# Kernel optimization log

Hardware: AMD Instinct MI355X
Metric: run time of the kernel (lower is better)

## Reference

```python
import jax, jax.numpy as jnp
import numpy as np

SCALE = 0.08838834764831845  # 1/sqrt(128)
SOFT_CAP = 0.0               # module default soft_cap=0 -> disabled


def setup_inputs() -> dict:
    key = jax.random.key(0)
    k1, k2, k3, k4, k5 = jax.random.split(key, 5)
    R, B, Hq, Hk, Dq, Dv = 4, 16, 32, 8, 128, 128
    P, PAGE, M = 8192, 1, 2048  # pages per rank, page_size, max pages per seq
    q = jax.random.normal(k1, (B, Hq, Dq), dtype=jnp.float16)
    k_cache = jax.random.normal(k2, (R, P, PAGE, Hk, Dq), dtype=jnp.float16)
    v_cache = jax.random.normal(k3, (R, P, PAGE, Hk, Dv), dtype=jnp.float16)
    # at least 1 valid token per rank per sequence
    global_kv_lens = jax.random.randint(k4, (R, B), 1, M * PAGE + 1, dtype=jnp.int32)
    block_table = jax.random.randint(k5, (R, B, M), 0, P, dtype=jnp.int32)
    return {"q": q, "k_cache": k_cache, "v_cache": v_cache,
            "global_kv_lens": global_kv_lens, "block_table": block_table}


def _flash_decode(q, k_cache, v_cache, global_kv_lens, block_table):
    R, P, PAGE, Hk, Dq = k_cache.shape
    B, Hq, _ = q.shape
    G = Hq // Hk                      # GQA group size
    M = block_table.shape[-1]
    K = M * PAGE                      # max kv tokens per rank per seq
    Dv = v_cache.shape[-1]

    # paged gather per rank: kc[bt] -> [B, M, PAGE, Hk, D]
    kg = jax.vmap(lambda kc, bt: kc[bt])(k_cache, block_table)
    vg = jax.vmap(lambda vc, bt: vc[bt])(v_cache, block_table)
    kg = kg.reshape(R, B, K, Hk, Dq).astype(jnp.float32)
    vg = vg.reshape(R, B, K, Hk, Dv).astype(jnp.float32)

    qf = q.astype(jnp.float32).reshape(B, Hk, G, Dq)
    # scores [R, B, Hk, G, K]
    s = jnp.einsum('bhgd,rbkhd->rbhgk', qf, kg) * SCALE
    if SOFT_CAP > 0:
        s = SOFT_CAP * jnp.tanh(s / SOFT_CAP)

    valid = jnp.arange(K)[None, None, :] < global_kv_lens[:, :, None]  # [R,B,K]
    s = jnp.where(valid[:, :, None, None, :], s, -jnp.inf)

    # per-rank partial softmax stats (what gqa_local_kernels_fused produces)
    m = jnp.max(s, axis=-1)                      # [R,B,Hk,G]
    p = jnp.exp(s - m[..., None])
    l = jnp.sum(p, axis=-1)                      # [R,B,Hk,G]
    o = jnp.einsum('rbhgk,rbkhd->rbhgd', p, vg)  # [R,B,Hk,G,Dv]

    # cross-rank lse-weighted reduce (gqa_global_reduce_fused)
    m_g = jnp.max(m, axis=0)                     # [B,Hk,G]
    w = jnp.exp(m - m_g[None])                   # [R,B,Hk,G]
    o_tot = jnp.sum(w[..., None] * o, axis=0)    # [B,Hk,G,Dv]
    l_tot = jnp.sum(w * l, axis=0)               # [B,Hk,G]
    out = (o_tot / l_tot[..., None]).reshape(B, Hq, Dv)
    return out.astype(jnp.float32)


def reference(q, k_cache, v_cache, global_kv_lens, block_table):
    return _flash_decode(q, k_cache, v_cache, global_kv_lens, block_table)
```

## Files before the change

### kernel.cpp

```cpp
#include <hip/hip_runtime.h>
#include <math.h>


typedef float f32x4 __attribute__((ext_vector_type(4)));

#define R_ 4
#define B_ 16
#define HQ_ 32
#define HK_ 8
#define G_ 4
#define D_ 128
#define P_ 8192
#define M_ 2048
#define HKD (HK_ * D_)
#define SC2 (0.08838834764831845f * 1.4426950408889634f)
#define MNEG (-1.0e30f)

__device__ __forceinline__ void load8u(const float* __restrict__ ubase,
                                       unsigned boff, float o[8]) {
  const f32x4* p = (const f32x4*)((const char*)ubase + boff);
  f32x4 a = p[0];
  f32x4 b = p[1];
#pragma unroll
  for (int j = 0; j < 4; ++j) { o[j] = a[j]; o[4 + j] = b[j]; }
}

__device__ __forceinline__ int clampP(int p) {
  return p < 0 ? 0 : (p >= P_ ? P_ - 1 : p);
}

__global__ __launch_bounds__(256) void fd_partial(
    const float* __restrict__ q, const float* __restrict__ kc,
    const float* __restrict__ vc, const int* __restrict__ lens,
    const int* __restrict__ bt, float* __restrict__ ws_m,
    float* __restrict__ ws_l, float* __restrict__ ws_o, int S) {
  const int idx = blockIdx.x;
  const int s = idx % S;
  const int hk = (idx / S) % HK_;
  const int b = (idx / (S * HK_)) % B_;
  const int r = idx / (S * HK_ * B_);

  const int lane = threadIdx.x & 63;
  const int w = threadIdx.x >> 6;
  const int tg = lane >> 4;
  const int ds = (lane & 15) * 8;
  const unsigned dsb = ds * 4u;
  const int rec = blockIdx.x;

  int kvlen = lens[r * B_ + b];
  if (kvlen < 0) kvlen = 0;
  if (kvlen > M_) kvlen = M_;
  const int chunk = (((kvlen + S - 1) / S) + 63) & ~63;
  const int t0 = s * chunk;
  int t1 = t0 + chunk;
  if (t1 > kvlen) t1 = kvlen;
  if (t0 >= t1) {
    if (lane == 0) ws_m[rec * G_ + w] = MNEG;
    return;
  }

  float qf[G_][8];
  {
    const float* qp = q + (size_t)(b * HQ_ + hk * G_) * D_ + ds;
#pragma unroll
    for (int h = 0; h < G_; ++h) {
      load8u(qp + h * D_, 0u, qf[h]);
#pragma unroll
      for (int j = 0; j < 8; ++j) qf[h][j] *= SC2;
    }
  }

  const int* btrow = bt + (r * B_ + b) * M_;
  const float* kb = kc + (size_t)r * P_ * HKD + (size_t)hk * D_;
  const float* vb = vc + (size_t)r * P_ * HKD + (size_t)hk * D_;

  float m[G_], l[G_], acc[G_][8];
#pragma unroll
  for (int h = 0; h < G_; ++h) {
    m[h] = MNEG;
    l[h] = 0.f;
#pragma unroll
    for (int j = 0; j < 8; ++j) acc[h][j] = 0.f;
  }

  const int nIter = (t1 - t0 + 63) >> 6;
  const int sbase = t0 + w * 16 + tg * 4;

  int4 pgN = *(const int4*)(btrow + sbase);

  for (int i = 0; i < nIter; ++i) {
    const int4 pg = pgN;
    if (i + 1 < nIter) pgN = *(const int4*)(btrow + sbase + (i + 1) * 64);
    const unsigned o0 = ((unsigned)clampP(pg.x) << 12) + dsb;
    const unsigned o1 = ((unsigned)clampP(pg.y) << 12) + dsb;
    const unsigned o2 = ((unsigned)clampP(pg.z) << 12) + dsb;
    const unsigned o3 = ((unsigned)clampP(pg.w) << 12) + dsb;

    float k0[8], k1[8], k2[8], k3[8], v0[8], v1[8], v2[8], v3[8];
    load8u(kb, o0, k0);
    load8u(kb, o1, k1);
    load8u(kb, o2, k2);
    load8u(kb, o3, k3);
    load8u(vb, o0, v0);
    load8u(vb, o1, v1);
    load8u(vb, o2, v2);
    load8u(vb, o3, v3);

    float d0[G_], d1[G_], d2[G_], d3[G_];
#pragma unroll
    for (int h = 0; h < G_; ++h) {
      float a0 = 0.f, a1 = 0.f, a2 = 0.f, a3 = 0.f;
#pragma unroll
      for (int j = 0; j < 8; ++j) {
        a0 += qf[h][j] * k0[j];
        a1 += qf[h][j] * k1[j];
        a2 += qf[h][j] * k2[j];
        a3 += qf[h][j] * k3[j];
      }
      d0[h] = a0; d1[h] = a1; d2[h] = a2; d3[h] = a3;
    }
#pragma unroll
    for (int msk = 1; msk <= 8; msk <<= 1) {
#pragma unroll
      for (int h = 0; h < G_; ++h) {
        d0[h] += __shfl_xor(d0[h], msk);
        d1[h] += __shfl_xor(d1[h], msk);
        d2[h] += __shfl_xor(d2[h], msk);
        d3[h] += __shfl_xor(d3[h], msk);
      }
    }

    const int tb = sbase + i * 64;
    const bool va0 = tb < t1;
    const bool va1 = tb + 1 < t1;
    const bool va2 = tb + 2 < t1;
    const bool va3 = tb + 3 < t1;
#pragma unroll
    for (int h = 0; h < G_; ++h) {
      const float s0 = va0 ? d0[h] : -INFINITY;
      const float s1 = va1 ? d1[h] : -INFINITY;
      const float s2 = va2 ? d2[h] : -INFINITY;
      const float s3 = va3 ? d3[h] : -INFINITY;
      const float mt = fmaxf(fmaxf(s0, s1), fmaxf(s2, s3));
      const float mn = fmaxf(m[h], mt);
      const float sc = exp2f(m[h] - mn);
      const float p0 = exp2f(s0 - mn);
      const float p1 = exp2f(s1 - mn);
      const float p2 = exp2f(s2 - mn);
      const float p3 = exp2f(s3 - mn);
      m[h] = mn;
      l[h] = l[h] * sc + (p0 + p1) + (p2 + p3);
#pragma unroll
      for (int j = 0; j < 8; ++j)
        acc[h][j] = acc[h][j] * sc + p0 * v0[j] + p1 * v1[j] + p2 * v2[j] +
                    p3 * v3[j];
    }
  }

#pragma unroll
  for (int h = 0; h < G_; ++h) {
#pragma unroll
    for (int off = 16; off <= 32; off <<= 1) {
      const float mo = __shfl_xor(m[h], off);
      const float lo = __shfl_xor(l[h], off);
      float ao[8];
#pragma unroll
      for (int j = 0; j < 8; ++j) ao[j] = __shfl_xor(acc[h][j], off);
      const float mn = fmaxf(m[h], mo);
      const float se = exp2f(m[h] - mn);
      const float so_ = exp2f(mo - mn);
      l[h] = l[h] * se + lo * so_;
#pragma unroll
      for (int j = 0; j < 8; ++j) acc[h][j] = acc[h][j] * se + ao[j] * so_;
      m[h] = mn;
    }
  }

  __shared__ float sm[4][G_], sl[4][G_], so[4][G_][D_ + 4];
  if (lane < 16) {
#pragma unroll
    for (int h = 0; h < G_; ++h) {
#pragma unroll
      for (int j = 0; j < 8; ++j) so[w][h][ds + j] = acc[h][j];
    }
    if (lane == 0) {
#pragma unroll
      for (int h = 0; h < G_; ++h) {
        sm[w][h] = m[h];
        sl[w][h] = l[h];
      }
    }
  }
  __syncthreads();

  const int g = w;
  const float mw0 = sm[0][g], mw1 = sm[1][g], mw2 = sm[2][g], mw3 = sm[3][g];
  const float mf = fmaxf(fmaxf(mw0, mw1), fmaxf(mw2, mw3));
  const float wt0 = exp2f(mw0 - mf);
  const float wt1 = exp2f(mw1 - mf);
  const float wt2 = exp2f(mw2 - mf);
  const float wt3 = exp2f(mw3 - mf);
  const float lf =
      wt0 * sl[0][g] + wt1 * sl[1][g] + wt2 * sl[2][g] + wt3 * sl[3][g];
  const float of0 = wt0 * so[0][g][lane] + wt1 * so[1][g][lane] +
                    wt2 * so[2][g][lane] + wt3 * so[3][g][lane];
  const float of1 = wt0 * so[0][g][lane + 64] + wt1 * so[1][g][lane + 64] +
                    wt2 * so[2][g][lane + 64] + wt3 * so[3][g][lane + 64];
  ws_o[((size_t)rec * G_ + g) * D_ + lane] = of0;
  ws_o[((size_t)rec * G_ + g) * D_ + lane + 64] = of1;
  if (lane == 0) {
    ws_m[rec * G_ + g] = mf;
    ws_l[rec * G_ + g] = lf;
  }
}

__global__ __launch_bounds__(128) void fd_reduce(
    const float* __restrict__ ws_m, const float* __restrict__ ws_l,
    const float* __restrict__ ws_o, float* __restrict__ out, int S) {
  const int row = blockIdx.x;
  const int g = row % G_;
  const int hk = (row / G_) % HK_;
  const int b = row / (G_ * HK_);
  const int d = threadIdx.x;

  float mf = MNEG;
  for (int r = 0; r < R_; ++r)
    for (int s = 0; s < S; ++s) {
      int rec = ((r * B_ + b) * HK_ + hk) * S + s;
      mf = fmaxf(mf, ws_m[rec * G_ + g]);
    }
  float of = 0.f, lf = 0.f;
  for (int r = 0; r < R_; ++r)
    for (int s = 0; s < S; ++s) {
      int rec = ((r * B_ + b) * HK_ + hk) * S + s;
      float wt = exp2f(ws_m[rec * G_ + g] - mf);
      of += wt * ws_o[((size_t)rec * G_ + g) * D_ + d];
      lf += wt * ws_l[rec * G_ + g];
    }
  out[(size_t)(b * HQ_ + hk * G_ + g) * D_ + d] = of / lf;
}

__global__ __launch_bounds__(256) void fd_mono(
    const float* __restrict__ q, const float* __restrict__ kc,
    const float* __restrict__ vc, const int* __restrict__ lens,
    const int* __restrict__ bt, float* __restrict__ out) {
  const int hk = blockIdx.x % HK_;
  const int b = blockIdx.x / HK_;
  const int lane = threadIdx.x & 63;
  const int g = threadIdx.x >> 6;
  const int tg = lane >> 4;
  const int ds = (lane & 15) * 8;
  const unsigned dsb = ds * 4u;

  float qf[8];
  load8u(q + (size_t)(b * HQ_ + hk * G_ + g) * D_ + ds, 0u, qf);
#pragma unroll
  for (int j = 0; j < 8; ++j) qf[j] *= SC2;

  float m = MNEG, l = 0.f, acc[8];
#pragma unroll
  for (int j = 0; j < 8; ++j) acc[j] = 0.f;

  for (int r = 0; r < R_; ++r) {
    int kvlen = lens[r * B_ + b];
    if (kvlen < 0) kvlen = 0;
    if (kvlen > M_) kvlen = M_;
    const int* btrow = bt + (r * B_ + b) * M_;
    const float* kb = kc + (size_t)r * P_ * HKD + (size_t)hk * D_;
    const float* vb = vc + (size_t)r * P_ * HKD + (size_t)hk * D_;

    for (int t = 0; t < kvlen; t += 4) {
      const int ta = t + tg;
      const bool va = ta < kvlen;
      const unsigned oa = ((unsigned)clampP(btrow[va ? ta : 0]) << 12) + dsb;
      float ka[8], wa[8];
      load8u(kb, oa, ka);
      load8u(vb, oa, wa);

      float da = 0.f;
#pragma unroll
      for (int j = 0; j < 8; ++j) da += qf[j] * ka[j];
#pragma unroll
      for (int msk = 1; msk <= 8; msk <<= 1) da += __shfl_xor(da, msk);

      const float sa = va ? da : -INFINITY;
      const float mn = fmaxf(m, sa);
      const float sc = exp2f(m - mn);
      const float pa = exp2f(sa - mn);
      m = mn;
      l = l * sc + pa;
#pragma unroll
      for (int j = 0; j < 8; ++j) acc[j] = acc[j] * sc + pa * wa[j];
    }
  }

#pragma unroll
  for (int off = 16; off <= 32; off <<= 1) {
    const float mo = __shfl_xor(m, off);
    const float lo = __shfl_xor(l, off);
    float ao[8];
#pragma unroll
    for (int j = 0; j < 8; ++j) ao[j] = __shfl_xor(acc[j], off);
    const float mn = fmaxf(m, mo);
    const float se = exp2f(m - mn);
    const float so_ = exp2f(mo - mn);
    l = l * se + lo * so_;
#pragma unroll
    for (int j = 0; j < 8; ++j) acc[j] = acc[j] * se + ao[j] * so_;
    m = mn;
  }

  if (lane < 16) {
    float inv = (l > 0.f) ? 1.0f / l : 0.f;
#pragma unroll
    for (int j = 0; j < 8; ++j)
      out[(size_t)(b * HQ_ + hk * G_ + g) * D_ + ds + j] = acc[j] * inv;
  }
}

extern "C" void kernel_launch(void* const* d_in, const int* in_sizes, int n_in,
                              void* d_out, int out_size, void* d_ws,
                              size_t ws_size, hipStream_t stream) {
  const float* q = (const float*)d_in[0];
  const float* kc = (const float*)d_in[1];
  const float* vc = (const float*)d_in[2];
  const int* lens = (const int*)d_in[3];
  const int* bt = (const int*)d_in[4];
  float* out = (float*)d_out;

  auto need = [](int s) {
    return (size_t)R_ * B_ * HK_ * s * (size_t)(2 * G_ + G_ * D_) *
           sizeof(float);
  };
  int S = 4;
  while (S > 1 && need(S) > ws_size) S >>= 1;

  if (need(S) <= ws_size) {
    const int nrec = R_ * B_ * HK_ * S;
    float* ws_m = (float*)d_ws;
    float* ws_l = ws_m + (size_t)nrec * G_;
    float* ws_o = ws_l + (size_t)nrec * G_;
    fd_partial<<<nrec, 256, 0, stream>>>(q, kc, vc, lens, bt, ws_m, ws_l,
                                         ws_o, S);
    fd_reduce<<<B_ * HK_ * G_, 128, 0, stream>>>(ws_m, ws_l, ws_o, out, S);
  } else {
    fd_mono<<<B_ * HK_, 256, 0, stream>>>(q, kc, vc, lens, bt, out);
  }
}
```

Baseline: 99.40 us.

## Split KV into fixed 128-token windows, one per wave, dropping in-block merge

Each wave now handles a fixed 128-token window (16 windows per rank/batch/head) rather than four waves sharing an adaptive chunk. This removes the shared-memory cross-wave merge and barrier, and windows past the sequence length exit early, which balances work across blocks. In exchange the workspace and the reduce kernel grow to 16 partial records per rank, and a larger workspace is required before falling back to the monolithic kernel.

Result: slower. 253.9 us (+155.4%).

```diff
diff --git a/kernel.cpp b/kernel.cpp
--- a/kernel.cpp
+++ b/kernel.cpp
@@ -13,6 +13,8 @@
 #define P_ 8192
 #define M_ 2048
 #define HKD (HK_ * D_)
+#define NWIN 16
+#define WTOK 128
 #define SC2 (0.08838834764831845f * 1.4426950408889634f)
 #define MNEG (-1.0e30f)
 
@@ -33,31 +35,31 @@
     const float* __restrict__ q, const float* __restrict__ kc,
     const float* __restrict__ vc, const int* __restrict__ lens,
     const int* __restrict__ bt, float* __restrict__ ws_m,
-    float* __restrict__ ws_l, float* __restrict__ ws_o, int S) {
-  const int idx = blockIdx.x;
-  const int s = idx % S;
-  const int hk = (idx / S) % HK_;
-  const int b = (idx / (S * HK_)) % B_;
-  const int r = idx / (S * HK_ * B_);
-
+    float* __restrict__ ws_l, float* __restrict__ ws_o) {
   const int lane = threadIdx.x & 63;
   const int w = threadIdx.x >> 6;
+  const int gw = blockIdx.x * 4 + w;
+  const int s = gw & (NWIN - 1);
+  const int hk = (gw >> 4) & (HK_ - 1);
+  const int b = (gw >> 7) & (B_ - 1);
+  const int r = gw >> 11;
+
   const int tg = lane >> 4;
   const int ds = (lane & 15) * 8;
   const unsigned dsb = ds * 4u;
-  const int rec = blockIdx.x;
 
   int kvlen = lens[r * B_ + b];
   if (kvlen < 0) kvlen = 0;
   if (kvlen > M_) kvlen = M_;
-  const int chunk = (((kvlen + S - 1) / S) + 63) & ~63;
-  const int t0 = s * chunk;
-  int t1 = t0 + chunk;
-  if (t1 > kvlen) t1 = kvlen;
-  if (t0 >= t1) {
-    if (lane == 0) ws_m[rec * G_ + w] = MNEG;
+  const int base = s * WTOK;
+  if (base >= kvlen) {
+    if (lane == 0) {
+#pragma unroll
+      for (int h = 0; h < G_; ++h) ws_m[gw * G_ + h] = MNEG;
+    }
     return;
   }
+  const int t1 = (base + WTOK < kvlen) ? base + WTOK : kvlen;
 
   float qf[G_][8];
   {
@@ -83,14 +85,13 @@
     for (int j = 0; j < 8; ++j) acc[h][j] = 0.f;
   }
 
-  const int nIter = (t1 - t0 + 63) >> 6;
-  const int sbase = t0 + w * 16 + tg * 4;
-
-  int4 pgN = *(const int4*)(btrow + sbase);
-
-  for (int i = 0; i < nIter; ++i) {
+  const int sstart = base + tg * 4;
+  int4 pgN = *(const int4*)(btrow + sstart);
+
+#pragma unroll
+  for (int i = 0; i < WTOK / 16; ++i) {
     const int4 pg = pgN;
-    if (i + 1 < nIter) pgN = *(const int4*)(btrow + sbase + (i + 1) * 64);
+    if (i + 1 < WTOK / 16) pgN = *(const int4*)(btrow + sstart + (i + 1) * 16);
     const unsigned o0 = ((unsigned)clampP(pg.x) << 12) + dsb;
     const unsigned o1 = ((unsigned)clampP(pg.y) << 12) + dsb;
     const unsigned o2 = ((unsigned)clampP(pg.z) << 12) + dsb;
@@ -130,7 +131,7 @@
       }
     }
 
-    const int tb = sbase + i * 64;
+    const int tb = sstart + i * 16;
     const bool va0 = tb < t1;
     const bool va1 = tb + 1 < t1;
     const bool va2 = tb + 2 < t1;
@@ -176,47 +177,26 @@
     }
   }
 
-  __shared__ float sm[4][G_], sl[4][G_], so[4][G_][D_ + 4];
   if (lane < 16) {
 #pragma unroll
     for (int h = 0; h < G_; ++h) {
 #pragma unroll
-      for (int j = 0; j < 8; ++j) so[w][h][ds + j] = acc[h][j];
-    }
-    if (lane == 0) {
-#pragma unroll
-      for (int h = 0; h < G_; ++h) {
-        sm[w][h] = m[h];
-        sl[w][h] = l[h];
-      }
-    }
-  }
-  __syncthreads();
-
-  const int g = w;
-  const float mw0 = sm[0][g], mw1 = sm[1][g], mw2 = sm[2][g], mw3 = sm[3][g];
-  const float mf = fmaxf(fmaxf(mw0, mw1), fmaxf(mw2, mw3));
-  const float wt0 = exp2f(mw0 - mf);
-  const float wt1 = exp2f(mw1 - mf);
-  const float wt2 = exp2f(mw2 - mf);
-  const float wt3 = exp2f(mw3 - mf);
-  const float lf =
-      wt0 * sl[0][g] + wt1 * sl[1][g] + wt2 * sl[2][g] + wt3 * sl[3][g];
-  const float of0 = wt0 * so[0][g][lane] + wt1 * so[1][g][lane] +
-                    wt2 * so[2][g][lane] + wt3 * so[3][g][lane];
-  const float of1 = wt0 * so[0][g][lane + 64] + wt1 * so[1][g][lane + 64] +
-                    wt2 * so[2][g][lane + 64] + wt3 * so[3][g][lane + 64];
-  ws_o[((size_t)rec * G_ + g) * D_ + lane] = of0;
-  ws_o[((size_t)rec * G_ + g) * D_ + lane + 64] = of1;
+      for (int j = 0; j < 8; ++j)
+        ws_o[((size_t)gw * G_ + h) * D_ + ds + j] = acc[h][j];
+    }
+  }
   if (lane == 0) {
-    ws_m[rec * G_ + g] = mf;
-    ws_l[rec * G_ + g] = lf;
+#pragma unroll
+    for (int h = 0; h < G_; ++h) {
+      ws_m[gw * G_ + h] = m[h];
+      ws_l[gw * G_ + h] = l[h];
+    }
   }
 }
 
 __global__ __launch_bounds__(128) void fd_reduce(
     const float* __restrict__ ws_m, const float* __restrict__ ws_l,
-    const float* __restrict__ ws_o, float* __restrict__ out, int S) {
+    const float* __restrict__ ws_o, float* __restrict__ out) {
   const int row = blockIdx.x;
   const int g = row % G_;
   const int hk = (row / G_) % HK_;
@@ -225,14 +205,14 @@
 
   float mf = MNEG;
   for (int r = 0; r < R_; ++r)
-    for (int s = 0; s < S; ++s) {
-      int rec = ((r * B_ + b) * HK_ + hk) * S + s;
+    for (int s = 0; s < NWIN; ++s) {
+      int rec = ((r * B_ + b) * HK_ + hk) * NWIN + s;
       mf = fmaxf(mf, ws_m[rec * G_ + g]);
     }
   float of = 0.f, lf = 0.f;
   for (int r = 0; r < R_; ++r)
-    for (int s = 0; s < S; ++s) {
-      int rec = ((r * B_ + b) * HK_ + hk) * S + s;
+    for (int s = 0; s < NWIN; ++s) {
+      int rec = ((r * B_ + b) * HK_ + hk) * NWIN + s;
       float wt = exp2f(ws_m[rec * G_ + g] - mf);
       of += wt * ws_o[((size_t)rec * G_ + g) * D_ + d];
       lf += wt * ws_l[rec * G_ + g];
@@ -328,21 +308,17 @@
   const int* bt = (const int*)d_in[4];
   float* out = (float*)d_out;
 
-  auto need = [](int s) {
-    return (size_t)R_ * B_ * HK_ * s * (size_t)(2 * G_ + G_ * D_) *
-           sizeof(float);
-  };
-  int S = 4;
-  while (S > 1 && need(S) > ws_size) S >>= 1;
-
-  if (need(S) <= ws_size) {
-    const int nrec = R_ * B_ * HK_ * S;
+  const int nrec = R_ * B_ * HK_ * NWIN;
+  const size_t need =
+      (size_t)nrec * (size_t)(2 * G_ + G_ * D_) * sizeof(float);
+
+  if (need <= ws_size) {
     float* ws_m = (float*)d_ws;
     float* ws_l = ws_m + (size_t)nrec * G_;
     float* ws_o = ws_l + (size_t)nrec * G_;
-    fd_partial<<<nrec, 256, 0, stream>>>(q, kc, vc, lens, bt, ws_m, ws_l,
-                                         ws_o, S);
-    fd_reduce<<<B_ * HK_ * G_, 128, 0, stream>>>(ws_m, ws_l, ws_o, out, S);
+    fd_partial<<<nrec / 4, 256, 0, stream>>>(q, kc, vc, lens, bt, ws_m, ws_l,
+                                             ws_o);
+    fd_reduce<<<B_ * HK_ * G_, 128, 0, stream>>>(ws_m, ws_l, ws_o, out);
   } else {
     fd_mono<<<B_ * HK_, 256, 0, stream>>>(q, kc, vc, lens, bt, out);
   }
```

## Bucket-sort page indices by page range so split-KV blocks share cache lines

Applied to the files above, without the earlier changes.

Adds a compaction kernel that counting-sorts each sequence's page indices into 8 page-address ranges, padding each range to a multiple of 64, and stores precomputed byte offsets. The partial kernel now launches 8 splits per (rank, batch, head), each working over pages from one address range, ordered split-major so concurrent blocks touch nearby memory. The aim is better L2 and TLB locality for the scattered paged gathers and more parallelism than the previous 4-way split. The cost is an extra kernel launch, a larger workspace, uneven work per split, and padded dummy entries that still get loaded before being masked.

Measured after the change: 100.6 us. Within noise of the previous version (+1.2%).

```diff
diff --git a/kernel.cpp b/kernel.cpp
--- a/kernel.cpp
+++ b/kernel.cpp
@@ -13,48 +13,90 @@
 #define P_ 8192
 #define M_ 2048
 #define HKD (HK_ * D_)
+#define NR 8
+#define NBK 256
+#define PROW 2560
 #define SC2 (0.08838834764831845f * 1.4426950408889634f)
 #define MNEG (-1.0e30f)
 
-__device__ __forceinline__ void load8u(const float* __restrict__ ubase,
-                                       unsigned boff, float o[8]) {
-  const f32x4* p = (const f32x4*)((const char*)ubase + boff);
-  f32x4 a = p[0];
-  f32x4 b = p[1];
-#pragma unroll
-  for (int j = 0; j < 4; ++j) { o[j] = a[j]; o[4 + j] = b[j]; }
-}
-
 __device__ __forceinline__ int clampP(int p) {
   return p < 0 ? 0 : (p >= P_ ? P_ - 1 : p);
 }
 
+__global__ __launch_bounds__(256) void fd_compact(
+    const int* __restrict__ lens, const int* __restrict__ bt,
+    unsigned* __restrict__ ws_pages, int* __restrict__ ws_meta) {
+  __shared__ int hist[NBK];
+  __shared__ int cur[NBK];
+  __shared__ int rstart[NR + 1], rcnt[NR];
+  const int rb = blockIdx.x;
+  const int tid = threadIdx.x;
+  int kvlen = lens[rb];
+  kvlen = kvlen < 0 ? 0 : (kvlen > M_ ? M_ : kvlen);
+  const int* btrow = bt + rb * M_;
+
+  for (int i = tid; i < NBK; i += 256) hist[i] = 0;
+  __syncthreads();
+  for (int t = tid; t < kvlen; t += 256)
+    atomicAdd(&hist[clampP(btrow[t]) >> 5], 1);
+  __syncthreads();
+  if (tid == 0) {
+    int pos = 0;
+    for (int s = 0; s < NR; ++s) {
+      rstart[s] = pos;
+      int n = 0;
+      for (int j = 0; j < NBK / NR; ++j) {
+        cur[s * (NBK / NR) + j] = pos + n;
+        n += hist[s * (NBK / NR) + j];
+      }
+      rcnt[s] = n;
+      pos += (n + 63) & ~63;
+    }
+    rstart[NR] = pos;
+  }
+  __syncthreads();
+  unsigned* prow = ws_pages + (size_t)rb * PROW;
+  for (int t = tid; t < kvlen; t += 256) {
+    const int p = clampP(btrow[t]);
+    const int d = atomicAdd(&cur[p >> 5], 1);
+    prow[d] = ((unsigned)p) << 12;
+  }
+  __syncthreads();
+  for (int s = 0; s < NR; ++s) {
+    const int from = rstart[s] + rcnt[s];
+    const int to = rstart[s + 1];
+    for (int i = from + tid; i < to; i += 256)
+      prow[i] = ((unsigned)(s * (P_ / NR))) << 12;
+  }
+  if (tid < NR) {
+    ws_meta[rb * 2 * NR + tid * 2] = rstart[tid];
+    ws_meta[rb * 2 * NR + tid * 2 + 1] = rcnt[tid];
+  }
+}
+
 __global__ __launch_bounds__(256) void fd_partial(
     const float* __restrict__ q, const float* __restrict__ kc,
-    const float* __restrict__ vc, const int* __restrict__ lens,
-    const int* __restrict__ bt, float* __restrict__ ws_m,
-    float* __restrict__ ws_l, float* __restrict__ ws_o, int S) {
-  const int idx = blockIdx.x;
-  const int s = idx % S;
-  const int hk = (idx / S) % HK_;
-  const int b = (idx / (S * HK_)) % B_;
-  const int r = idx / (S * HK_ * B_);
+    const float* __restrict__ vc, const unsigned* __restrict__ ws_pages,
+    const int* __restrict__ ws_meta, float* __restrict__ ws_m,
+    float* __restrict__ ws_l, float* __restrict__ ws_o) {
+  const int bid = blockIdx.x;
+  const int s = bid >> 9;
+  const int rbh = bid & 511;
+  const int hk = rbh & (HK_ - 1);
+  const int rb = rbh >> 3;
+  const int b = rb & (B_ - 1);
+  const int r = rb >> 4;
+  const int rec = bid;
 
   const int lane = threadIdx.x & 63;
   const int w = threadIdx.x >> 6;
   const int tg = lane >> 4;
   const int ds = (lane & 15) * 8;
   const unsigned dsb = ds * 4u;
-  const int rec = blockIdx.x;
-
-  int kvlen = lens[r * B_ + b];
-  if (kvlen < 0) kvlen = 0;
-  if (kvlen > M_) kvlen = M_;
-  const int chunk = (((kvlen + S - 1) / S) + 63) & ~63;
-  const int t0 = s * chunk;
-  int t1 = t0 + chunk;
-  if (t1 > kvlen) t1 = kvlen;
-  if (t0 >= t1) {
+
+  const int start = ws_meta[rb * 2 * NR + s * 2];
+  const int n = ws_meta[rb * 2 * NR + s * 2 + 1];
+  if (n <= 0) {
     if (lane == 0) ws_m[rec * G_ + w] = MNEG;
     return;
   }
@@ -64,13 +106,17 @@
     const float* qp = q + (size_t)(b * HQ_ + hk * G_) * D_ + ds;
 #pragma unroll
     for (int h = 0; h < G_; ++h) {
-      load8u(qp + h * D_, 0u, qf[h]);
-#pragma unroll
-      for (int j = 0; j < 8; ++j) qf[h][j] *= SC2;
-    }
-  }
-
-  const int* btrow = bt + (r * B_ + b) * M_;
+      const f32x4* p = (const f32x4*)(qp + h * D_);
+      f32x4 a = p[0], c = p[1];
+#pragma unroll
+      for (int j = 0; j < 4; ++j) {
+        qf[h][j] = a[j] * SC2;
+        qf[h][4 + j] = c[j] * SC2;
+      }
+    }
+  }
+
+  const unsigned* plist = ws_pages + (size_t)rb * PROW + start;
   const float* kb = kc + (size_t)r * P_ * HKD + (size_t)hk * D_;
   const float* vb = vc + (size_t)r * P_ * HKD + (size_t)hk * D_;
 
@@ -83,28 +129,50 @@
     for (int j = 0; j < 8; ++j) acc[h][j] = 0.f;
   }
 
-  const int nIter = (t1 - t0 + 63) >> 6;
-  const int sbase = t0 + w * 16 + tg * 4;
-
-  int4 pgN = *(const int4*)(btrow + sbase);
-
-  for (int i = 0; i < nIter; ++i) {
-    const int4 pg = pgN;
-    if (i + 1 < nIter) pgN = *(const int4*)(btrow + sbase + (i + 1) * 64);
-    const unsigned o0 = ((unsigned)clampP(pg.x) << 12) + dsb;
-    const unsigned o1 = ((unsigned)clampP(pg.y) << 12) + dsb;
-    const unsigned o2 = ((unsigned)clampP(pg.z) << 12) + dsb;
-    const unsigned o3 = ((unsigned)clampP(pg.w) << 12) + dsb;
+  const int nIt = (n + 63) >> 6;
+  const int sbase = w * 16 + tg * 4;
+
+  uint4 pgN = *(const uint4*)(plist + sbase);
+
+#pragma unroll 1
+  for (int i = 0; i < nIt; ++i) {
+    const uint4 pg = pgN;
+    if (i + 1 < nIt) pgN = *(const uint4*)(plist + sbase + (i + 1) * 64);
+    const unsigned o0 = pg.x + dsb;
+    const unsigned o1 = pg.y + dsb;
+    const unsigned o2 = pg.z + dsb;
+    const unsigned o3 = pg.w + dsb;
 
     float k0[8], k1[8], k2[8], k3[8], v0[8], v1[8], v2[8], v3[8];
-    load8u(kb, o0, k0);
-    load8u(kb, o1, k1);
-    load8u(kb, o2, k2);
-    load8u(kb, o3, k3);
-    load8u(vb, o0, v0);
-    load8u(vb, o1, v1);
-    load8u(vb, o2, v2);
-    load8u(vb, o3, v3);
+    {
+      const char* kcb = (const char*)kb;
+      const char* vcb = (const char*)vb;
+      const f32x4* p;
+      p = (const f32x4*)(kcb + o0);
+#pragma unroll
+      for (int j = 0; j < 4; ++j) { k0[j] = p[0][j]; k0[4 + j] = p[1][j]; }
+      p = (const f32x4*)(kcb + o1);
+#pragma unroll
+      for (int j = 0; j < 4; ++j) { k1[j] = p[0][j]; k1[4 + j] = p[1][j]; }
+      p = (const f32x4*)(kcb + o2);
+#pragma unroll
+      for (int j = 0; j < 4; ++j) { k2[j] = p[0][j]; k2[4 + j] = p[1][j]; }
+      p = (const f32x4*)(kcb + o3);
+#pragma unroll
+      for (int j = 0; j < 4; ++j) { k3[j] = p[0][j]; k3[4 + j] = p[1][j]; }
+      p = (const f32x4*)(vcb + o0);
+#pragma unroll
+      for (int j = 0; j < 4; ++j) { v0[j] = p[0][j]; v0[4 + j] = p[1][j]; }
+      p = (const f32x4*)(vcb + o1);
+#pragma unroll
+      for (int j = 0; j < 4; ++j) { v1[j] = p[0][j]; v1[4 + j] = p[1][j]; }
+      p = (const f32x4*)(vcb + o2);
+#pragma unroll
+      for (int j = 0; j < 4; ++j) { v2[j] = p[0][j]; v2[4 + j] = p[1][j]; }
+      p = (const f32x4*)(vcb + o3);
+#pragma unroll
+      for (int j = 0; j < 4; ++j) { v3[j] = p[0][j]; v3[4 + j] = p[1][j]; }
+    }
 
     float d0[G_], d1[G_], d2[G_], d3[G_];
 #pragma unroll
@@ -131,10 +199,10 @@
     }
 
     const int tb = sbase + i * 64;
-    const bool va0 = tb < t1;
-    const bool va1 = tb + 1 < t1;
-    const bool va2 = tb + 2 < t1;
-    const bool va3 = tb + 3 < t1;
+    const bool va0 = tb < n;
+    const bool va1 = tb + 1 < n;
+    const bool va2 = tb + 2 < n;
+    const bool va3 = tb + 3 < n;
 #pragma unroll
     for (int h = 0; h < G_; ++h) {
       const float s0 = va0 ? d0[h] : -INFINITY;
@@ -216,7 +284,7 @@
 
 __global__ __launch_bounds__(128) void fd_reduce(
     const float* __restrict__ ws_m, const float* __restrict__ ws_l,
-    const float* __restrict__ ws_o, float* __restrict__ out, int S) {
+    const float* __restrict__ ws_o, float* __restrict__ out) {
   const int row = blockIdx.x;
   const int g = row % G_;
   const int hk = (row / G_) % HK_;
@@ -225,19 +293,28 @@
 
   float mf = MNEG;
   for (int r = 0; r < R_; ++r)
-    for (int s = 0; s < S; ++s) {
-      int rec = ((r * B_ + b) * HK_ + hk) * S + s;
+    for (int s = 0; s < NR; ++s) {
+      const int rec = s * 512 + (r * B_ + b) * HK_ + hk;
       mf = fmaxf(mf, ws_m[rec * G_ + g]);
     }
   float of = 0.f, lf = 0.f;
   for (int r = 0; r < R_; ++r)
-    for (int s = 0; s < S; ++s) {
-      int rec = ((r * B_ + b) * HK_ + hk) * S + s;
-      float wt = exp2f(ws_m[rec * G_ + g] - mf);
+    for (int s = 0; s < NR; ++s) {
+      const int rec = s * 512 + (r * B_ + b) * HK_ + hk;
+      const float wt = exp2f(ws_m[rec * G_ + g] - mf);
       of += wt * ws_o[((size_t)rec * G_ + g) * D_ + d];
       lf += wt * ws_l[rec * G_ + g];
     }
   out[(size_t)(b * HQ_ + hk * G_ + g) * D_ + d] = of / lf;
+}
+
+__device__ __forceinline__ void load8u(const float* __restrict__ ubase,
+                                       unsigned boff, float o[8]) {
+  const f32x4* p = (const f32x4*)((const char*)ubase + boff);
+  f32x4 a = p[0];
+  f32x4 b = p[1];
+#pragma unroll
+  for (int j = 0; j < 4; ++j) { o[j] = a[j]; o[4 + j] = b[j]; }
 }
 
 __global__ __launch_bounds__(256) void fd_mono(
@@ -269,6 +346,7 @@
     const float* kb = kc + (size_t)r * P_ * HKD + (size_t)hk * D_;
     const float* vb = vc + (size_t)r * P_ * HKD + (size_t)hk * D_;
 
+#pragma unroll 1
     for (int t = 0; t < kvlen; t += 4) {
       const int ta = t + tg;
       const bool va = ta < kvlen;
@@ -328,21 +406,24 @@
   const int* bt = (const int*)d_in[4];
   float* out = (float*)d_out;
 
-  auto need = [](int s) {
-    return (size_t)R_ * B_ * HK_ * s * (size_t)(2 * G_ + G_ * D_) *
-           sizeof(float);
-  };
-  int S = 4;
-  while (S > 1 && need(S) > ws_size) S >>= 1;
-
-  if (need(S) <= ws_size) {
-    const int nrec = R_ * B_ * HK_ * S;
-    float* ws_m = (float*)d_ws;
-    float* ws_l = ws_m + (size_t)nrec * G_;
-    float* ws_o = ws_l + (size_t)nrec * G_;
-    fd_partial<<<nrec, 256, 0, stream>>>(q, kc, vc, lens, bt, ws_m, ws_l,
-                                         ws_o, S);
-    fd_reduce<<<B_ * HK_ * G_, 128, 0, stream>>>(ws_m, ws_l, ws_o, out, S);
+  const int nrec = NR * R_ * B_ * HK_;
+  const size_t sz_pages = (size_t)R_ * B_ * PROW * 4;
+  const size_t sz_meta = (size_t)R_ * B_ * 2 * NR * 4;
+  const size_t sz_ml = (size_t)nrec * G_ * 4;
+  const size_t sz_o = (size_t)nrec * G_ * D_ * 4;
+  const size_t need = sz_pages + sz_meta + 2 * sz_ml + sz_o;
+
+  if (need <= ws_size) {
+    char* p = (char*)d_ws;
+    unsigned* ws_pages = (unsigned*)p;          p += sz_pages;
+    int* ws_meta = (int*)p;                     p += sz_meta;
+    float* ws_m = (float*)p;                    p += sz_ml;
+    float* ws_l = (float*)p;                    p += sz_ml;
+    float* ws_o = (float*)p;
+    fd_compact<<<R_ * B_, 256, 0, stream>>>(lens, bt, ws_pages, ws_meta);
+    fd_partial<<<nrec, 256, 0, stream>>>(q, kc, vc, ws_pages, ws_meta, ws_m,
+                                         ws_l, ws_o);
+    fd_reduce<<<B_ * HK_ * G_, 128, 0, stream>>>(ws_m, ws_l, ws_o, out);
   } else {
     fd_mono<<<B_ * HK_, 256, 0, stream>>>(q, kc, vc, lens, bt, out);
   }
```
